# Optimization experiments

Hardware: AMD Instinct MI355X
Metric: run time of the kernel (lower is better)

Reference implementation:

```python
import jax, jax.numpy as jnp
import numpy as np

HEAD_SIZE = 64

def setup_inputs() -> dict:
    key = jax.random.key(0)
    k1, k2, k3, k4 = jax.random.split(key, 4)
    B, T, D = 4, 4096, 768
    x = jax.random.normal(k1, (B, T, D), dtype=jnp.float32)
    Wq = jax.random.normal(k2, (D, HEAD_SIZE), dtype=jnp.float32) * (1.0 / np.sqrt(D))
    Wk = jax.random.normal(k3, (D, HEAD_SIZE), dtype=jnp.float32) * (1.0 / np.sqrt(D))
    Wv = jax.random.normal(k4, (D, HEAD_SIZE), dtype=jnp.float32) * (1.0 / np.sqrt(D))
    return {"x": x, "Wq": Wq, "Wk": Wk, "Wv": Wv}

def reference(x, Wq, Wk, Wv):
    # q,k,v: [B, T, H]
    q = jnp.einsum('btd,dh->bth', x, Wq)
    k = jnp.einsum('btd,dh->bth', x, Wk)
    v = jnp.einsum('btd,dh->bth', x, Wv)
    # scores: [B, T, T]; causal mask via lower-triangular band, -inf elsewhere
    scores = jnp.einsum('bqh,bkh->bqk', q, k)
    T = x.shape[1]
    causal = jnp.tril(jnp.ones((T, T), dtype=bool))  # band_part(ones, -1, 0)
    scores = jnp.where(causal[None, :, :], scores, -jnp.inf)
    attn = jax.nn.softmax(scores / np.sqrt(HEAD_SIZE), axis=-1)
    # dropout is identity in eval mode
    return jnp.einsum('bqk,bkh->bqh', attn, v)
```

## Files before the change

### kernel.cpp

```cpp
#include <hip/hip_runtime.h>
#include <math.h>

typedef __attribute__((ext_vector_type(8))) short short8;
typedef __attribute__((ext_vector_type(4))) float f32x4;
typedef unsigned short ushort_t;

#define TSEQ   4096
#define NBATCH 4
#define DMODEL 768
#define HS     64
#define KSPLIT 8

static __device__ __forceinline__ ushort_t f2bf(float f) {
  union { float f; unsigned u; } v; v.f = f;
  unsigned r = v.u + 0x7fffu + ((v.u >> 16) & 1u);
  return (ushort_t)(r >> 16);
}
static __device__ __forceinline__ float bf2f(ushort_t u) {
  union { unsigned u; float f; } v; v.u = ((unsigned)u) << 16; return v.f;
}

#define MFMA16(a,b,c) __builtin_amdgcn_mfma_f32_16x16x32_bf16((a),(b),(c),0,0,0)

__global__ __launch_bounds__(256) void wprep(
    const float* __restrict__ Wq, const float* __restrict__ Wk,
    const float* __restrict__ Wv, ushort_t* __restrict__ Wt)
{
  __shared__ float lds[64 * 65];
  const int m = blockIdx.x / 12, kc = blockIdx.x % 12, k0 = kc * 64;
  const float* W = (m == 0) ? Wq : (m == 1) ? Wk : Wv;
  const int tid = threadIdx.x;
#pragma unroll
  for (int i = 0; i < 16; i++) {
    const int row = i * 4 + (tid >> 6), col = tid & 63;
    lds[row * 65 + col] = W[(size_t)(k0 + row) * HS + col];
  }
  __syncthreads();
#pragma unroll
  for (int i = 0; i < 16; i++) {
    const int n = i * 4 + (tid >> 6), kk = tid & 63;
    Wt[(size_t)(m * 64 + n) * DMODEL + k0 + kk] = f2bf(lds[kk * 65 + n]);
  }
}

__global__ __launch_bounds__(256, 2) void qkv_mfma(
    const float* __restrict__ x, const ushort_t* __restrict__ Wt,
    ushort_t* __restrict__ q, ushort_t* __restrict__ kO, ushort_t* __restrict__ vT)
{
  __shared__ __align__(16) ushort_t sA[2][32 * 72];
  __shared__ __align__(16) ushort_t sB[2][192 * 64];

  const int tid  = threadIdx.x;
  const int w    = tid >> 6;
  const int lane = tid & 63;
  const int l16  = lane & 15, quad = lane >> 4;
  const int M0   = blockIdx.x * 32;

  const int arow = tid >> 3, acol = (tid & 7) * 8;
  const float* ax = x + (size_t)(M0 + arow) * DMODEL + acol;

  const int bcol_l = lane >> 3;
  const int bkoff  = (((lane & 7) ^ (bcol_l & 7)) << 3);

  f32x4 acc[2][3];
#pragma unroll
  for (int mt = 0; mt < 2; mt++)
#pragma unroll
    for (int nt = 0; nt < 3; nt++) acc[mt][nt] = (f32x4){0.f, 0.f, 0.f, 0.f};

  {
#pragma unroll
    for (int j = 0; j < 6; j++) {
      const int colb = w * 48 + j * 8;
      __builtin_amdgcn_global_load_lds(
          (const __attribute__((address_space(1))) ushort_t*)
              (Wt + (size_t)(colb + bcol_l) * DMODEL + bkoff),
          (__attribute__((address_space(3))) ushort_t*)(&sB[0][colb * 64]),
          16, 0, 0);
    }
    const float4 f0 = *(const float4*)(ax);
    const float4 f1 = *(const float4*)(ax + 4);
    short8 p;
    p[0]=f2bf(f0.x); p[1]=f2bf(f0.y); p[2]=f2bf(f0.z); p[3]=f2bf(f0.w);
    p[4]=f2bf(f1.x); p[5]=f2bf(f1.y); p[6]=f2bf(f1.z); p[7]=f2bf(f1.w);
    *(short8*)(&sA[0][arow * 72 + acol]) = p;
  }

  for (int ks = 0; ks < DMODEL / 64; ks++) {
    const int cur = ks & 1, nxt = cur ^ 1;
    __syncthreads();

    float4 f0n, f1n;
    if (ks < DMODEL / 64 - 1) {
#pragma unroll
      for (int j = 0; j < 6; j++) {
        const int colb = w * 48 + j * 8;
        __builtin_amdgcn_global_load_lds(
            (const __attribute__((address_space(1))) ushort_t*)
                (Wt + (size_t)(colb + bcol_l) * DMODEL + (ks + 1) * 64 + bkoff),
            (__attribute__((address_space(3))) ushort_t*)(&sB[nxt][colb * 64]),
            16, 0, 0);
      }
      f0n = *(const float4*)(ax + (ks + 1) * 64);
      f1n = *(const float4*)(ax + (ks + 1) * 64 + 4);
    }

    const ushort_t* sAc = &sA[cur][0];
    const ushort_t* sBc = &sB[cur][0];
#pragma unroll
    for (int kc = 0; kc < 2; kc++) {
      const short8 a0 = *(const short8*)(sAc + (l16)      * 72 + kc * 32 + quad * 8);
      const short8 a1 = *(const short8*)(sAc + (16 + l16) * 72 + kc * 32 + quad * 8);
      const int kswz = (kc * 32 + quad * 8) ^ ((l16 & 7) << 3);
#pragma unroll
      for (int nt = 0; nt < 3; nt++) {
        const short8 bf =
            *(const short8*)(sBc + (w * 48 + nt * 16 + l16) * 64 + kswz);
        acc[0][nt] = MFMA16(a0, bf, acc[0][nt]);
        acc[1][nt] = MFMA16(a1, bf, acc[1][nt]);
      }
    }

    if (ks < DMODEL / 64 - 1) {
      short8 p;
      p[0]=f2bf(f0n.x); p[1]=f2bf(f0n.y); p[2]=f2bf(f0n.z); p[3]=f2bf(f0n.w);
      p[4]=f2bf(f1n.x); p[5]=f2bf(f1n.y); p[6]=f2bf(f1n.z); p[7]=f2bf(f1n.w);
      *(short8*)(&sA[nxt][arow * 72 + acol]) = p;
    }
  }

#pragma unroll
  for (int mt = 0; mt < 2; mt++)
#pragma unroll
    for (int nt = 0; nt < 3; nt++) {
      const int gnt = w * 3 + nt;
      const int mat = gnt >> 2;
      if (mat == 0) {
        const int col = (gnt & 3) * 16 + l16;
#pragma unroll
        for (int r = 0; r < 4; r++)
          q[(size_t)(M0 + mt * 16 + quad * 4 + r) * HS + col] =
              f2bf(acc[mt][nt][r] * 0.125f);
      } else if (mat == 1) {
        const int cb2 = (gnt & 3) * 2 + (l16 >> 3);
#pragma unroll
        for (int r = 0; r < 4; r++) {
          const int trow  = M0 + mt * 16 + quad * 4 + r;
          const int cphys = ((cb2 ^ (trow & 7)) << 3) | (l16 & 7);
          kO[(size_t)trow * HS + cphys] = f2bf(acc[mt][nt][r]);
        }
      }
    }
  __syncthreads();
  float* vls = (float*)&sA[0][0];
#pragma unroll
  for (int mt = 0; mt < 2; mt++)
#pragma unroll
    for (int nt = 0; nt < 3; nt++) {
      const int gnt = w * 3 + nt;
      if ((gnt >> 2) == 2) {
        const int vcol = (gnt & 3) * 16 + l16;
#pragma unroll
        for (int r = 0; r < 4; r++)
          vls[(mt * 16 + quad * 4 + r) * 65 + vcol] = acc[mt][nt][r];
      }
    }
  __syncthreads();
  const int d = tid >> 2, seg = tid & 3;
  short8 pk;
#pragma unroll
  for (int i = 0; i < 8; i++) pk[i] = (short)f2bf(vls[(seg * 8 + i) * 65 + d]);
  {
    const int t0  = M0 & (TSEQ - 1);
    const int tb  = t0 & ~63;
    const int kb  = ((t0 & 63) >> 3) + seg;
    const int kbp = kb ^ (d & 7);
    *(short8*)(vT + ((size_t)(M0 >> 12) * HS + d) * TSEQ + tb + kbp * 8) = pk;
  }
}

__global__ __launch_bounds__(256, 4) void attn_part(
    const ushort_t* __restrict__ q, const ushort_t* __restrict__ k,
    const ushort_t* __restrict__ vT, float* __restrict__ ML, ushort_t* __restrict__ OP)
{
  __shared__ __align__(16) ushort_t sK[2][64 * 64];
  __shared__ __align__(16) ushort_t sV[2][64 * 64];
  __shared__ __align__(16) ushort_t sP[4][16 * 64];

  const int idx  = blockIdx.x;
  const int s    = idx & 7;
  const int b    = (idx >> 3) & 3;
  const int jp   = idx >> 5;
  const int tid  = threadIdx.x;
  const int w    = tid >> 6;
  const int lane = tid & 63;
  const int l16  = lane & 15, quad = lane >> 4;

  const ushort_t* qg = q  + (size_t)b * TSEQ * HS;
  const ushort_t* kg = k  + (size_t)b * TSEQ * HS;
  const ushort_t* vg = vT + (size_t)b * HS * TSEQ;

  const int srow = lane >> 3;
  const int scol = (lane & 7) * 8;

#pragma unroll
  for (int h = 0; h < 2; h++) {
    const int j  = h ? jp : (63 - jp);
    const int R0 = j * 64 + w * 16;

    const short8 qf0 = *(const short8*)(qg + (size_t)(R0 + l16) * HS +      quad * 8);
    const short8 qf1 = *(const short8*)(qg + (size_t)(R0 + l16) * HS + 32 + quad * 8);

    f32x4 o[4];
#pragma unroll
    for (int dt = 0; dt < 4; dt++) o[dt] = (f32x4){0.f, 0.f, 0.f, 0.f};
    float mrow = -INFINITY, lrow = 0.f;

    const int nkt = j + 1;
    int kt = s, cur = 0;
    if (h) __syncthreads();
    if (kt < nkt) {
      const int k0 = kt * 64;
#pragma unroll
      for (int jj = 0; jj < 2; jj++) {
        const int r0 = w * 16 + jj * 8;
        __builtin_amdgcn_global_load_lds(
            (const __attribute__((address_space(1))) ushort_t*)
                (kg + (size_t)(k0 + r0 + srow) * HS + scol),
            (__attribute__((address_space(3))) ushort_t*)(&sK[0][r0 * 64]),
            16, 0, 0);
        __builtin_amdgcn_global_load_lds(
            (const __attribute__((address_space(1))) ushort_t*)
                (vg + (size_t)(r0 + srow) * TSEQ + k0 + scol),
            (__attribute__((address_space(3))) ushort_t*)(&sV[0][r0 * 64]),
            16, 0, 0);
      }
    }
    for (; kt < nkt; kt += KSPLIT) {
      const int k0 = kt * 64;
      __syncthreads();
      if (kt + KSPLIT < nkt) {
        const int kn = (kt + KSPLIT) * 64;
#pragma unroll
        for (int jj = 0; jj < 2; jj++) {
          const int r0 = w * 16 + jj * 8;
          __builtin_amdgcn_global_load_lds(
              (const __attribute__((address_space(1))) ushort_t*)
                  (kg + (size_t)(kn + r0 + srow) * HS + scol),
              (__attribute__((address_space(3))) ushort_t*)(&sK[cur ^ 1][r0 * 64]),
              16, 0, 0);
          __builtin_amdgcn_global_load_lds(
              (const __attribute__((address_space(1))) ushort_t*)
                  (vg + (size_t)(r0 + srow) * TSEQ + kn + scol),
              (__attribute__((address_space(3))) ushort_t*)(&sV[cur ^ 1][r0 * 64]),
              16, 0, 0);
        }
      }
      const ushort_t* sKc = &sK[cur][0];
      const ushort_t* sVc = &sV[cur][0];
      const int sw = (l16 & 7) << 3;

      f32x4 sT[4];
      __builtin_amdgcn_s_setprio(1);
#pragma unroll
      for (int ct = 0; ct < 4; ct++) {
        sT[ct] = (f32x4){0.f, 0.f, 0.f, 0.f};
        const short8 kfa = *(const short8*)(sKc + (ct * 16 + l16) * 64 + ((quad * 8)      ^ sw));
        const short8 kfb = *(const short8*)(sKc + (ct * 16 + l16) * 64 + ((32 + quad * 8) ^ sw));
        sT[ct] = MFMA16(kfa, qf0, sT[ct]);
        sT[ct] = MFMA16(kfb, qf1, sT[ct]);
      }
      __builtin_amdgcn_s_setprio(0);
      if (k0 + 63 > R0) {
        const int qrow = R0 + l16;
#pragma unroll
        for (int ct = 0; ct < 4; ct++)
#pragma unroll
          for (int r = 0; r < 4; r++)
            sT[ct][r] = (k0 + ct * 16 + quad * 4 + r <= qrow) ? sT[ct][r] : -INFINITY;
      }
      float tm = -INFINITY;
#pragma unroll
      for (int ct = 0; ct < 4; ct++)
#pragma unroll
        for (int r = 0; r < 4; r++) tm = fmaxf(tm, sT[ct][r]);
      tm = fmaxf(tm, __shfl_xor(tm, 16));
      tm = fmaxf(tm, __shfl_xor(tm, 32));
      const float mn = fmaxf(mrow, tm);
      const float al = __expf(mrow - mn);
      mrow = mn;
      float ps = 0.f;
#pragma unroll
      for (int ct = 0; ct < 4; ct++)
#pragma unroll
        for (int r = 0; r < 4; r++) { sT[ct][r] = __expf(sT[ct][r] - mn); ps += sT[ct][r]; }
      ps += __shfl_xor(ps, 16);
      ps += __shfl_xor(ps, 32);
      lrow = lrow * al + ps;
      ushort_t* Pw = &sP[w][0];
#pragma unroll
      for (int ct = 0; ct < 4; ct++) {
        ushort4 pk;
        pk.x = f2bf(sT[ct][0]); pk.y = f2bf(sT[ct][1]);
        pk.z = f2bf(sT[ct][2]); pk.w = f2bf(sT[ct][3]);
        const int pb = (ct * 2 + (quad >> 1)) ^ (l16 & 7);
        *(ushort4*)(Pw + l16 * 64 + pb * 8 + (quad & 1) * 4) = pk;
      }
      float alo[4];
#pragma unroll
      for (int r = 0; r < 4; r++) alo[r] = __shfl(al, quad * 4 + r);
#pragma unroll
      for (int dt = 0; dt < 4; dt++)
#pragma unroll
        for (int r = 0; r < 4; r++) o[dt][r] *= alo[r];
      const short8 pf0 = *(const short8*)(Pw + l16 * 64 + (((quad)     ^ (l16 & 7)) << 3));
      const short8 pf1 = *(const short8*)(Pw + l16 * 64 + (((4 + quad) ^ (l16 & 7)) << 3));
      __builtin_amdgcn_s_setprio(1);
#pragma unroll
      for (int dt = 0; dt < 4; dt++) {
        const short8 vfa = *(const short8*)(sVc + (dt * 16 + l16) * 64 + ((quad * 8)      ^ sw));
        const short8 vfb = *(const short8*)(sVc + (dt * 16 + l16) * 64 + ((32 + quad * 8) ^ sw));
        o[dt] = MFMA16(pf0, vfa, o[dt]);
        o[dt] = MFMA16(pf1, vfb, o[dt]);
      }
      __builtin_amdgcn_s_setprio(0);
      cur ^= 1;
    }

    const size_t base = ((size_t)(b * KSPLIT + s) * TSEQ);
    if (quad == 0) {
      ML[(base + R0 + l16) * 2 + 0] = mrow;
      ML[(base + R0 + l16) * 2 + 1] = lrow;
    }
#pragma unroll
    for (int dt = 0; dt < 4; dt++)
#pragma unroll
      for (int r = 0; r < 4; r++)
        OP[(base + R0 + quad * 4 + r) * HS + dt * 16 + l16] = f2bf(o[dt][r]);
  }
}

__global__ __launch_bounds__(256) void attn_merge(
    const float* __restrict__ ML, const ushort_t* __restrict__ OP,
    float* __restrict__ out)
{
  const int row = blockIdx.x * 16 + (threadIdx.x >> 4);
  const int b   = row >> 12, t = row & (TSEQ - 1);
  const int d0  = (threadIdx.x & 15) * 4;
  float m[KSPLIT], l[KSPLIT];
  float M = -INFINITY;
#pragma unroll
  for (int ss = 0; ss < KSPLIT; ss++) {
    const size_t i = ((size_t)(b * KSPLIT + ss) * TSEQ + t);
    m[ss] = ML[i * 2]; l[ss] = ML[i * 2 + 1];
    M = fmaxf(M, m[ss]);
  }
  float den = 0.f;
  float4 num = make_float4(0.f, 0.f, 0.f, 0.f);
#pragma unroll
  for (int ss = 0; ss < KSPLIT; ss++) {
    const float a = __expf(m[ss] - M);
    den += l[ss] * a;
    const size_t i = ((size_t)(b * KSPLIT + ss) * TSEQ + t);
    const ushort4 u = *(const ushort4*)(OP + i * HS + d0);
    num.x += a * bf2f(u.x); num.y += a * bf2f(u.y);
    num.z += a * bf2f(u.z); num.w += a * bf2f(u.w);
  }
  const float inv = 1.f / den;
  *(float4*)(out + (size_t)row * HS + d0) =
      make_float4(num.x * inv, num.y * inv, num.z * inv, num.w * inv);
}

extern "C" void kernel_launch(void* const* d_in, const int* in_sizes, int n_in,
                              void* d_out, int out_size, void* d_ws, size_t ws_size,
                              hipStream_t stream) {
  const float* x  = (const float*)d_in[0];
  const float* Wq = (const float*)d_in[1];
  const float* Wk = (const float*)d_in[2];
  const float* Wv = (const float*)d_in[3];
  float* out = (float*)d_out;

  char* ws = (char*)d_ws;
  ushort_t* Wt = (ushort_t*)ws;
  ushort_t* qb = (ushort_t*)(ws + 294912);
  ushort_t* kb = (ushort_t*)(ws + 294912 + 2097152);
  ushort_t* vb = (ushort_t*)(ws + 294912 + 2 * 2097152);
  float*    ml = (float*)   (ws + 294912 + 3 * 2097152);
  ushort_t* op = (ushort_t*)(ws + 294912 + 3 * 2097152 + 1048576);

  wprep<<<36, 256, 0, stream>>>(Wq, Wk, Wv, Wt);
  qkv_mfma<<<(NBATCH * TSEQ) / 32, 256, 0, stream>>>(x, Wt, qb, kb, vb);
  attn_part<<<32 * NBATCH * KSPLIT, 256, 0, stream>>>(qb, kb, vb, ml, op);
  attn_merge<<<1024, 256, 0, stream>>>(ml, op, out);
}
```

Baseline: 131.3 us.

## Fuse all four kernels into one cooperative kernel with grid syncs

```diff
diff --git a/kernel.cpp b/kernel.cpp
--- a/kernel.cpp
+++ b/kernel.cpp
@@ -1,5 +1,8 @@
 #include <hip/hip_runtime.h>
+#include <hip/hip_cooperative_groups.h>
 #include <math.h>
+
+namespace cg = cooperative_groups;
 
 typedef __attribute__((ext_vector_type(8))) short short8;
 typedef __attribute__((ext_vector_type(4))) float f32x4;
@@ -9,7 +12,7 @@
 #define NBATCH 4
 #define DMODEL 768
 #define HS     64
-#define KSPLIT 8
+#define KS     4
 
 static __device__ __forceinline__ ushort_t f2bf(float f) {
   union { float f; unsigned u; } v; v.f = f;
@@ -22,353 +25,360 @@
 
 #define MFMA16(a,b,c) __builtin_amdgcn_mfma_f32_16x16x32_bf16((a),(b),(c),0,0,0)
 
-__global__ __launch_bounds__(256) void wprep(
-    const float* __restrict__ Wq, const float* __restrict__ Wk,
-    const float* __restrict__ Wv, ushort_t* __restrict__ Wt)
+__global__ __launch_bounds__(256, 2) void fused_all(
+    const float* __restrict__ x,  const float* __restrict__ Wq,
+    const float* __restrict__ Wk, const float* __restrict__ Wv,
+    ushort_t* __restrict__ Wt, ushort_t* __restrict__ q,
+    ushort_t* __restrict__ kO, ushort_t* __restrict__ vT,
+    float* __restrict__ ML, ushort_t* __restrict__ OP,
+    float* __restrict__ out)
 {
-  __shared__ float lds[64 * 65];
-  const int m = blockIdx.x / 12, kc = blockIdx.x % 12, k0 = kc * 64;
-  const float* W = (m == 0) ? Wq : (m == 1) ? Wk : Wv;
-  const int tid = threadIdx.x;
-#pragma unroll
-  for (int i = 0; i < 16; i++) {
-    const int row = i * 4 + (tid >> 6), col = tid & 63;
-    lds[row * 65 + col] = W[(size_t)(k0 + row) * HS + col];
-  }
-  __syncthreads();
-#pragma unroll
-  for (int i = 0; i < 16; i++) {
-    const int n = i * 4 + (tid >> 6), kk = tid & 63;
-    Wt[(size_t)(m * 64 + n) * DMODEL + k0 + kk] = f2bf(lds[kk * 65 + n]);
-  }
-}
-
-__global__ __launch_bounds__(256, 2) void qkv_mfma(
-    const float* __restrict__ x, const ushort_t* __restrict__ Wt,
-    ushort_t* __restrict__ q, ushort_t* __restrict__ kO, ushort_t* __restrict__ vT)
-{
-  __shared__ __align__(16) ushort_t sA[2][32 * 72];
-  __shared__ __align__(16) ushort_t sB[2][192 * 64];
+  __shared__ __align__(16) ushort_t smem[29184];
+
+  cg::grid_group grid = cg::this_grid();
 
   const int tid  = threadIdx.x;
+  const int bid  = blockIdx.x;
   const int w    = tid >> 6;
   const int lane = tid & 63;
   const int l16  = lane & 15, quad = lane >> 4;
-  const int M0   = blockIdx.x * 32;
-
-  const int arow = tid >> 3, acol = (tid & 7) * 8;
-  const float* ax = x + (size_t)(M0 + arow) * DMODEL + acol;
-
-  const int bcol_l = lane >> 3;
-  const int bkoff  = (((lane & 7) ^ (bcol_l & 7)) << 3);
-
-  f32x4 acc[2][3];
-#pragma unroll
-  for (int mt = 0; mt < 2; mt++)
-#pragma unroll
-    for (int nt = 0; nt < 3; nt++) acc[mt][nt] = (f32x4){0.f, 0.f, 0.f, 0.f};
+
+  if (bid < 36) {
+    float* lds = (float*)smem;
+    const int m = bid / 12, kc = bid % 12, k0 = kc * 64;
+    const float* W = (m == 0) ? Wq : (m == 1) ? Wk : Wv;
+#pragma unroll
+    for (int i = 0; i < 16; i++) {
+      const int row = i * 4 + (tid >> 6), col = tid & 63;
+      lds[row * 65 + col] = W[(size_t)(k0 + row) * HS + col];
+    }
+    __syncthreads();
+#pragma unroll
+    for (int i = 0; i < 16; i++) {
+      const int n = i * 4 + (tid >> 6), kk = tid & 63;
+      Wt[(size_t)(m * 64 + n) * DMODEL + k0 + kk] = f2bf(lds[kk * 65 + n]);
+    }
+  }
+  grid.sync();
 
   {
-#pragma unroll
-    for (int j = 0; j < 6; j++) {
-      const int colb = w * 48 + j * 8;
-      __builtin_amdgcn_global_load_lds(
-          (const __attribute__((address_space(1))) ushort_t*)
-              (Wt + (size_t)(colb + bcol_l) * DMODEL + bkoff),
-          (__attribute__((address_space(3))) ushort_t*)(&sB[0][colb * 64]),
-          16, 0, 0);
-    }
-    const float4 f0 = *(const float4*)(ax);
-    const float4 f1 = *(const float4*)(ax + 4);
-    short8 p;
-    p[0]=f2bf(f0.x); p[1]=f2bf(f0.y); p[2]=f2bf(f0.z); p[3]=f2bf(f0.w);
-    p[4]=f2bf(f1.x); p[5]=f2bf(f1.y); p[6]=f2bf(f1.z); p[7]=f2bf(f1.w);
-    *(short8*)(&sA[0][arow * 72 + acol]) = p;
-  }
-
-  for (int ks = 0; ks < DMODEL / 64; ks++) {
-    const int cur = ks & 1, nxt = cur ^ 1;
-    __syncthreads();
-
-    float4 f0n, f1n;
-    if (ks < DMODEL / 64 - 1) {
+    ushort_t* sA = smem;
+    ushort_t* sB = smem + 2 * 32 * 72;
+    const int M0 = bid * 32;
+
+    const int arow = tid >> 3, acol = (tid & 7) * 8;
+    const float* ax = x + (size_t)(M0 + arow) * DMODEL + acol;
+
+    const int bcol_l = lane >> 3;
+    const int bkoff  = (((lane & 7) ^ (bcol_l & 7)) << 3);
+
+    f32x4 acc[2][3];
+#pragma unroll
+    for (int mt = 0; mt < 2; mt++)
+#pragma unroll
+      for (int nt = 0; nt < 3; nt++) acc[mt][nt] = (f32x4){0.f, 0.f, 0.f, 0.f};
+
+    {
 #pragma unroll
       for (int j = 0; j < 6; j++) {
         const int colb = w * 48 + j * 8;
         __builtin_amdgcn_global_load_lds(
             (const __attribute__((address_space(1))) ushort_t*)
-                (Wt + (size_t)(colb + bcol_l) * DMODEL + (ks + 1) * 64 + bkoff),
-            (__attribute__((address_space(3))) ushort_t*)(&sB[nxt][colb * 64]),
+                (Wt + (size_t)(colb + bcol_l) * DMODEL + bkoff),
+            (__attribute__((address_space(3))) ushort_t*)(&sB[colb * 64]),
             16, 0, 0);
       }
-      f0n = *(const float4*)(ax + (ks + 1) * 64);
-      f1n = *(const float4*)(ax + (ks + 1) * 64 + 4);
-    }
-
-    const ushort_t* sAc = &sA[cur][0];
-    const ushort_t* sBc = &sB[cur][0];
-#pragma unroll
-    for (int kc = 0; kc < 2; kc++) {
-      const short8 a0 = *(const short8*)(sAc + (l16)      * 72 + kc * 32 + quad * 8);
-      const short8 a1 = *(const short8*)(sAc + (16 + l16) * 72 + kc * 32 + quad * 8);
-      const int kswz = (kc * 32 + quad * 8) ^ ((l16 & 7) << 3);
+      const float4 f0 = *(const float4*)(ax);
+      const float4 f1 = *(const float4*)(ax + 4);
+      short8 p;
+      p[0]=f2bf(f0.x); p[1]=f2bf(f0.y); p[2]=f2bf(f0.z); p[3]=f2bf(f0.w);
+      p[4]=f2bf(f1.x); p[5]=f2bf(f1.y); p[6]=f2bf(f1.z); p[7]=f2bf(f1.w);
+      *(short8*)(&sA[arow * 72 + acol]) = p;
+    }
+
+    for (int ks = 0; ks < DMODEL / 64; ks++) {
+      const int cur = ks & 1, nxt = cur ^ 1;
+      __syncthreads();
+
+      float4 f0n, f1n;
+      if (ks < DMODEL / 64 - 1) {
+#pragma unroll
+        for (int j = 0; j < 6; j++) {
+          const int colb = w * 48 + j * 8;
+          __builtin_amdgcn_global_load_lds(
+              (const __attribute__((address_space(1))) ushort_t*)
+                  (Wt + (size_t)(colb + bcol_l) * DMODEL + (ks + 1) * 64 + bkoff),
+              (__attribute__((address_space(3))) ushort_t*)
+                  (&sB[nxt * 192 * 64 + colb * 64]),
+              16, 0, 0);
+        }
+        f0n = *(const float4*)(ax + (ks + 1) * 64);
+        f1n = *(const float4*)(ax + (ks + 1) * 64 + 4);
+      }
+
+      const ushort_t* sAc = &sA[cur * 32 * 72];
+      const ushort_t* sBc = &sB[cur * 192 * 64];
+#pragma unroll
+      for (int kc = 0; kc < 2; kc++) {
+        const short8 a0 = *(const short8*)(sAc + (l16)      * 72 + kc * 32 + quad * 8);
+        const short8 a1 = *(const short8*)(sAc + (16 + l16) * 72 + kc * 32 + quad * 8);
+        const int kswz = (kc * 32 + quad * 8) ^ ((l16 & 7) << 3);
+#pragma unroll
+        for (int nt = 0; nt < 3; nt++) {
+          const short8 bf =
+              *(const short8*)(sBc + (w * 48 + nt * 16 + l16) * 64 + kswz);
+          acc[0][nt] = MFMA16(a0, bf, acc[0][nt]);
+          acc[1][nt] = MFMA16(a1, bf, acc[1][nt]);
+        }
+      }
+
+      if (ks < DMODEL / 64 - 1) {
+        short8 p;
+        p[0]=f2bf(f0n.x); p[1]=f2bf(f0n.y); p[2]=f2bf(f0n.z); p[3]=f2bf(f0n.w);
+        p[4]=f2bf(f1n.x); p[5]=f2bf(f1n.y); p[6]=f2bf(f1n.z); p[7]=f2bf(f1n.w);
+        *(short8*)(&sA[nxt * 32 * 72 + arow * 72 + acol]) = p;
+      }
+    }
+
+#pragma unroll
+    for (int mt = 0; mt < 2; mt++)
 #pragma unroll
       for (int nt = 0; nt < 3; nt++) {
-        const short8 bf =
-            *(const short8*)(sBc + (w * 48 + nt * 16 + l16) * 64 + kswz);
-        acc[0][nt] = MFMA16(a0, bf, acc[0][nt]);
-        acc[1][nt] = MFMA16(a1, bf, acc[1][nt]);
-      }
-    }
-
-    if (ks < DMODEL / 64 - 1) {
-      short8 p;
-      p[0]=f2bf(f0n.x); p[1]=f2bf(f0n.y); p[2]=f2bf(f0n.z); p[3]=f2bf(f0n.w);
-      p[4]=f2bf(f1n.x); p[5]=f2bf(f1n.y); p[6]=f2bf(f1n.z); p[7]=f2bf(f1n.w);
-      *(short8*)(&sA[nxt][arow * 72 + acol]) = p;
+        const int gnt = w * 3 + nt;
+        const int mat = gnt >> 2;
+        if (mat == 0) {
+          const int col = (gnt & 3) * 16 + l16;
+#pragma unroll
+          for (int r = 0; r < 4; r++)
+            q[(size_t)(M0 + mt * 16 + quad * 4 + r) * HS + col] =
+                f2bf(acc[mt][nt][r] * 0.125f);
+        } else if (mat == 1) {
+          const int cb2 = (gnt & 3) * 2 + (l16 >> 3);
+#pragma unroll
+          for (int r = 0; r < 4; r++) {
+            const int trow  = M0 + mt * 16 + quad * 4 + r;
+            const int cphys = ((cb2 ^ (trow & 7)) << 3) | (l16 & 7);
+            kO[(size_t)trow * HS + cphys] = f2bf(acc[mt][nt][r]);
+          }
+        }
+      }
+    __syncthreads();
+    float* vls = (float*)smem;
+#pragma unroll
+    for (int mt = 0; mt < 2; mt++)
+#pragma unroll
+      for (int nt = 0; nt < 3; nt++) {
+        const int gnt = w * 3 + nt;
+        if ((gnt >> 2) == 2) {
+          const int vcol = (gnt & 3) * 16 + l16;
+#pragma unroll
+          for (int r = 0; r < 4; r++)
+            vls[(mt * 16 + quad * 4 + r) * 65 + vcol] = acc[mt][nt][r];
+        }
+      }
+    __syncthreads();
+    const int d = tid >> 2, seg = tid & 3;
+    short8 pk;
+#pragma unroll
+    for (int i = 0; i < 8; i++) pk[i] = (short)f2bf(vls[(seg * 8 + i) * 65 + d]);
+    {
+      const int t0  = M0 & (TSEQ - 1);
+      const int tb  = t0 & ~63;
+      const int kb  = ((t0 & 63) >> 3) + seg;
+      const int kbp = kb ^ (d & 7);
+      *(short8*)(vT + ((size_t)(M0 >> 12) * HS + d) * TSEQ + tb + kbp * 8) = pk;
     }
   }
-
-#pragma unroll
-  for (int mt = 0; mt < 2; mt++)
-#pragma unroll
-    for (int nt = 0; nt < 3; nt++) {
-      const int gnt = w * 3 + nt;
-      const int mat = gnt >> 2;
-      if (mat == 0) {
-        const int col = (gnt & 3) * 16 + l16;
-#pragma unroll
-        for (int r = 0; r < 4; r++)
-          q[(size_t)(M0 + mt * 16 + quad * 4 + r) * HS + col] =
-              f2bf(acc[mt][nt][r] * 0.125f);
-      } else if (mat == 1) {
-        const int cb2 = (gnt & 3) * 2 + (l16 >> 3);
-#pragma unroll
-        for (int r = 0; r < 4; r++) {
-          const int trow  = M0 + mt * 16 + quad * 4 + r;
-          const int cphys = ((cb2 ^ (trow & 7)) << 3) | (l16 & 7);
-          kO[(size_t)trow * HS + cphys] = f2bf(acc[mt][nt][r]);
-        }
-      }
-    }
-  __syncthreads();
-  float* vls = (float*)&sA[0][0];
-#pragma unroll
-  for (int mt = 0; mt < 2; mt++)
-#pragma unroll
-    for (int nt = 0; nt < 3; nt++) {
-      const int gnt = w * 3 + nt;
-      if ((gnt >> 2) == 2) {
-        const int vcol = (gnt & 3) * 16 + l16;
-#pragma unroll
-        for (int r = 0; r < 4; r++)
-          vls[(mt * 16 + quad * 4 + r) * 65 + vcol] = acc[mt][nt][r];
-      }
-    }
-  __syncthreads();
-  const int d = tid >> 2, seg = tid & 3;
-  short8 pk;
-#pragma unroll
-  for (int i = 0; i < 8; i++) pk[i] = (short)f2bf(vls[(seg * 8 + i) * 65 + d]);
+  grid.sync();
+
   {
-    const int t0  = M0 & (TSEQ - 1);
-    const int tb  = t0 & ~63;
-    const int kb  = ((t0 & 63) >> 3) + seg;
-    const int kbp = kb ^ (d & 7);
-    *(short8*)(vT + ((size_t)(M0 >> 12) * HS + d) * TSEQ + tb + kbp * 8) = pk;
-  }
-}
-
-__global__ __launch_bounds__(256, 4) void attn_part(
-    const ushort_t* __restrict__ q, const ushort_t* __restrict__ k,
-    const ushort_t* __restrict__ vT, float* __restrict__ ML, ushort_t* __restrict__ OP)
-{
-  __shared__ __align__(16) ushort_t sK[2][64 * 64];
-  __shared__ __align__(16) ushort_t sV[2][64 * 64];
-  __shared__ __align__(16) ushort_t sP[4][16 * 64];
-
-  const int idx  = blockIdx.x;
-  const int s    = idx & 7;
-  const int b    = (idx >> 3) & 3;
-  const int jp   = idx >> 5;
-  const int tid  = threadIdx.x;
-  const int w    = tid >> 6;
-  const int lane = tid & 63;
-  const int l16  = lane & 15, quad = lane >> 4;
-
-  const ushort_t* qg = q  + (size_t)b * TSEQ * HS;
-  const ushort_t* kg = k  + (size_t)b * TSEQ * HS;
-  const ushort_t* vg = vT + (size_t)b * HS * TSEQ;
-
-  const int srow = lane >> 3;
-  const int scol = (lane & 7) * 8;
-
-#pragma unroll
-  for (int h = 0; h < 2; h++) {
-    const int j  = h ? jp : (63 - jp);
-    const int R0 = j * 64 + w * 16;
-
-    const short8 qf0 = *(const short8*)(qg + (size_t)(R0 + l16) * HS +      quad * 8);
-    const short8 qf1 = *(const short8*)(qg + (size_t)(R0 + l16) * HS + 32 + quad * 8);
-
-    f32x4 o[4];
-#pragma unroll
-    for (int dt = 0; dt < 4; dt++) o[dt] = (f32x4){0.f, 0.f, 0.f, 0.f};
-    float mrow = -INFINITY, lrow = 0.f;
-
-    const int nkt = j + 1;
-    int kt = s, cur = 0;
-    if (h) __syncthreads();
-    if (kt < nkt) {
-      const int k0 = kt * 64;
-#pragma unroll
-      for (int jj = 0; jj < 2; jj++) {
-        const int r0 = w * 16 + jj * 8;
-        __builtin_amdgcn_global_load_lds(
-            (const __attribute__((address_space(1))) ushort_t*)
-                (kg + (size_t)(k0 + r0 + srow) * HS + scol),
-            (__attribute__((address_space(3))) ushort_t*)(&sK[0][r0 * 64]),
-            16, 0, 0);
-        __builtin_amdgcn_global_load_lds(
-            (const __attribute__((address_space(1))) ushort_t*)
-                (vg + (size_t)(r0 + srow) * TSEQ + k0 + scol),
-            (__attribute__((address_space(3))) ushort_t*)(&sV[0][r0 * 64]),
-            16, 0, 0);
-      }
-    }
-    for (; kt < nkt; kt += KSPLIT) {
-      const int k0 = kt * 64;
-      __syncthreads();
-      if (kt + KSPLIT < nkt) {
-        const int kn = (kt + KSPLIT) * 64;
+    ushort_t* sK = smem;
+    ushort_t* sV = smem + 2 * 64 * 64;
+    ushort_t* sP = smem + 4 * 64 * 64;
+
+    const int s  = bid & 3;
+    const int b  = (bid >> 2) & 3;
+    const int jp = bid >> 4;
+
+    const ushort_t* qg = q  + (size_t)b * TSEQ * HS;
+    const ushort_t* kg = kO + (size_t)b * TSEQ * HS;
+    const ushort_t* vg = vT + (size_t)b * HS * TSEQ;
+
+    const int srow = lane >> 3;
+    const int scol = (lane & 7) * 8;
+
+#pragma unroll
+    for (int h = 0; h < 2; h++) {
+      const int j  = h ? jp : (63 - jp);
+      const int R0 = j * 64 + w * 16;
+
+      const short8 qf0 = *(const short8*)(qg + (size_t)(R0 + l16) * HS +      quad * 8);
+      const short8 qf1 = *(const short8*)(qg + (size_t)(R0 + l16) * HS + 32 + quad * 8);
+
+      f32x4 o[4];
+#pragma unroll
+      for (int dt = 0; dt < 4; dt++) o[dt] = (f32x4){0.f, 0.f, 0.f, 0.f};
+      float mrow = -INFINITY, lrow = 0.f;
+
+      const int nkt = j + 1;
+      int kt = s, cur = 0;
+      if (h) __syncthreads();
+      if (kt < nkt) {
+        const int k0 = kt * 64;
 #pragma unroll
         for (int jj = 0; jj < 2; jj++) {
           const int r0 = w * 16 + jj * 8;
           __builtin_amdgcn_global_load_lds(
               (const __attribute__((address_space(1))) ushort_t*)
-                  (kg + (size_t)(kn + r0 + srow) * HS + scol),
-              (__attribute__((address_space(3))) ushort_t*)(&sK[cur ^ 1][r0 * 64]),
+                  (kg + (size_t)(k0 + r0 + srow) * HS + scol),
+              (__attribute__((address_space(3))) ushort_t*)(&sK[r0 * 64]),
               16, 0, 0);
           __builtin_amdgcn_global_load_lds(
               (const __attribute__((address_space(1))) ushort_t*)
-                  (vg + (size_t)(r0 + srow) * TSEQ + kn + scol),
-              (__attribute__((address_space(3))) ushort_t*)(&sV[cur ^ 1][r0 * 64]),
+                  (vg + (size_t)(r0 + srow) * TSEQ + k0 + scol),
+              (__attribute__((address_space(3))) ushort_t*)(&sV[r0 * 64]),
               16, 0, 0);
         }
       }
-      const ushort_t* sKc = &sK[cur][0];
-      const ushort_t* sVc = &sV[cur][0];
-      const int sw = (l16 & 7) << 3;
-
-      f32x4 sT[4];
-      __builtin_amdgcn_s_setprio(1);
-#pragma unroll
-      for (int ct = 0; ct < 4; ct++) {
-        sT[ct] = (f32x4){0.f, 0.f, 0.f, 0.f};
-        const short8 kfa = *(const short8*)(sKc + (ct * 16 + l16) * 64 + ((quad * 8)      ^ sw));
-        const short8 kfb = *(const short8*)(sKc + (ct * 16 + l16) * 64 + ((32 + quad * 8) ^ sw));
-        sT[ct] = MFMA16(kfa, qf0, sT[ct]);
-        sT[ct] = MFMA16(kfb, qf1, sT[ct]);
-      }
-      __builtin_amdgcn_s_setprio(0);
-      if (k0 + 63 > R0) {
-        const int qrow = R0 + l16;
+      for (; kt < nkt; kt += KS) {
+        const int k0 = kt * 64;
+        __syncthreads();
+        if (kt + KS < nkt) {
+          const int kn = (kt + KS) * 64;
+#pragma unroll
+          for (int jj = 0; jj < 2; jj++) {
+            const int r0 = w * 16 + jj * 8;
+            __builtin_amdgcn_global_load_lds(
+                (const __attribute__((address_space(1))) ushort_t*)
+                    (kg + (size_t)(kn + r0 + srow) * HS + scol),
+                (__attribute__((address_space(3))) ushort_t*)
+                    (&sK[(cur ^ 1) * 64 * 64 + r0 * 64]),
+                16, 0, 0);
+            __builtin_amdgcn_global_load_lds(
+                (const __attribute__((address_space(1))) ushort_t*)
+                    (vg + (size_t)(r0 + srow) * TSEQ + kn + scol),
+                (__attribute__((address_space(3))) ushort_t*)
+                    (&sV[(cur ^ 1) * 64 * 64 + r0 * 64]),
+                16, 0, 0);
+          }
+        }
+        const ushort_t* sKc = &sK[cur * 64 * 64];
+        const ushort_t* sVc = &sV[cur * 64 * 64];
+        const int sw = (l16 & 7) << 3;
+
+        f32x4 sT[4];
+        __builtin_amdgcn_s_setprio(1);
+#pragma unroll
+        for (int ct = 0; ct < 4; ct++) {
+          sT[ct] = (f32x4){0.f, 0.f, 0.f, 0.f};
+          const short8 kfa = *(const short8*)(sKc + (ct * 16 + l16) * 64 + ((quad * 8)      ^ sw));
+          const short8 kfb = *(const short8*)(sKc + (ct * 16 + l16) * 64 + ((32 + quad * 8) ^ sw));
+          sT[ct] = MFMA16(kfa, qf0, sT[ct]);
+          sT[ct] = MFMA16(kfb, qf1, sT[ct]);
+        }
+        __builtin_amdgcn_s_setprio(0);
+        if (k0 + 63 > R0) {
+          const int qrow = R0 + l16;
+#pragma unroll
+          for (int ct = 0; ct < 4; ct++)
+#pragma unroll
+            for (int r = 0; r < 4; r++)
+              sT[ct][r] = (k0 + ct * 16 + quad * 4 + r <= qrow) ? sT[ct][r] : -INFINITY;
+        }
+        float tm = -INFINITY;
 #pragma unroll
         for (int ct = 0; ct < 4; ct++)
 #pragma unroll
-          for (int r = 0; r < 4; r++)
-            sT[ct][r] = (k0 + ct * 16 + quad * 4 + r <= qrow) ? sT[ct][r] : -INFINITY;
-      }
-      float tm = -INFINITY;
-#pragma unroll
-      for (int ct = 0; ct < 4; ct++)
-#pragma unroll
-        for (int r = 0; r < 4; r++) tm = fmaxf(tm, sT[ct][r]);
-      tm = fmaxf(tm, __shfl_xor(tm, 16));
-      tm = fmaxf(tm, __shfl_xor(tm, 32));
-      const float mn = fmaxf(mrow, tm);
-      const float al = __expf(mrow - mn);
-      mrow = mn;
-      float ps = 0.f;
-#pragma unroll
-      for (int ct = 0; ct < 4; ct++)
-#pragma unroll
-        for (int r = 0; r < 4; r++) { sT[ct][r] = __expf(sT[ct][r] - mn); ps += sT[ct][r]; }
-      ps += __shfl_xor(ps, 16);
-      ps += __shfl_xor(ps, 32);
-      lrow = lrow * al + ps;
-      ushort_t* Pw = &sP[w][0];
-#pragma unroll
-      for (int ct = 0; ct < 4; ct++) {
-        ushort4 pk;
-        pk.x = f2bf(sT[ct][0]); pk.y = f2bf(sT[ct][1]);
-        pk.z = f2bf(sT[ct][2]); pk.w = f2bf(sT[ct][3]);
-        const int pb = (ct * 2 + (quad >> 1)) ^ (l16 & 7);
-        *(ushort4*)(Pw + l16 * 64 + pb * 8 + (quad & 1) * 4) = pk;
-      }
-      float alo[4];
-#pragma unroll
-      for (int r = 0; r < 4; r++) alo[r] = __shfl(al, quad * 4 + r);
+          for (int r = 0; r < 4; r++) tm = fmaxf(tm, sT[ct][r]);
+        tm = fmaxf(tm, __shfl_xor(tm, 16));
+        tm = fmaxf(tm, __shfl_xor(tm, 32));
+        const float mn = fmaxf(mrow, tm);
+        const float al = __expf(mrow - mn);
+        mrow = mn;
+        float ps = 0.f;
+#pragma unroll
+        for (int ct = 0; ct < 4; ct++)
+#pragma unroll
+          for (int r = 0; r < 4; r++) { sT[ct][r] = __expf(sT[ct][r] - mn); ps += sT[ct][r]; }
+        ps += __shfl_xor(ps, 16);
+        ps += __shfl_xor(ps, 32);
+        lrow = lrow * al + ps;
+
+        ushort_t* Pw = &sP[w * 16 * 64];
+#pragma unroll
+        for (int ct = 0; ct < 4; ct++) {
+          ushort4 pk;
+          pk.x = f2bf(sT[ct][0]); pk.y = f2bf(sT[ct][1]);
+          pk.z = f2bf(sT[ct][2]); pk.w = f2bf(sT[ct][3]);
+          const int pb = (ct * 2 + (quad >> 1)) ^ (l16 & 7);
+          *(ushort4*)(Pw + l16 * 64 + pb * 8 + (quad & 1) * 4) = pk;
+        }
+        float alo[4];
+#pragma unroll
+        for (int r = 0; r < 4; r++) alo[r] = __shfl(al, quad * 4 + r);
+#pragma unroll
+        for (int dt = 0; dt < 4; dt++)
+#pragma unroll
+          for (int r = 0; r < 4; r++) o[dt][r] *= alo[r];
+        const short8 pf0 = *(const short8*)(Pw + l16 * 64 + (((quad)     ^ (l16 & 7)) << 3));
+        const short8 pf1 = *(const short8*)(Pw + l16 * 64 + (((4 + quad) ^ (l16 & 7)) << 3));
+        __builtin_amdgcn_s_setprio(1);
+#pragma unroll
+        for (int dt = 0; dt < 4; dt++) {
+          const short8 vfa = *(const short8*)(sVc + (dt * 16 + l16) * 64 + ((quad * 8)      ^ sw));
+          const short8 vfb = *(const short8*)(sVc + (dt * 16 + l16) * 64 + ((32 + quad * 8) ^ sw));
+          o[dt] = MFMA16(pf0, vfa, o[dt]);
+          o[dt] = MFMA16(pf1, vfb, o[dt]);
+        }
+        __builtin_amdgcn_s_setprio(0);
+        cur ^= 1;
+      }
+
+      const size_t base = ((size_t)(b * KS + s) * TSEQ);
+      if (quad == 0) {
+        ML[(base + R0 + l16) * 2 + 0] = mrow;
+        ML[(base + R0 + l16) * 2 + 1] = lrow;
+      }
 #pragma unroll
       for (int dt = 0; dt < 4; dt++)
 #pragma unroll
-        for (int r = 0; r < 4; r++) o[dt][r] *= alo[r];
-      const short8 pf0 = *(const short8*)(Pw + l16 * 64 + (((quad)     ^ (l16 & 7)) << 3));
-      const short8 pf1 = *(const short8*)(Pw + l16 * 64 + (((4 + quad) ^ (l16 & 7)) << 3));
-      __builtin_amdgcn_s_setprio(1);
-#pragma unroll
-      for (int dt = 0; dt < 4; dt++) {
-        const short8 vfa = *(const short8*)(sVc + (dt * 16 + l16) * 64 + ((quad * 8)      ^ sw));
-        const short8 vfb = *(const short8*)(sVc + (dt * 16 + l16) * 64 + ((32 + quad * 8) ^ sw));
-        o[dt] = MFMA16(pf0, vfa, o[dt]);
-        o[dt] = MFMA16(pf1, vfb, o[dt]);
-      }
-      __builtin_amdgcn_s_setprio(0);
-      cur ^= 1;
-    }
-
-    const size_t base = ((size_t)(b * KSPLIT + s) * TSEQ);
-    if (quad == 0) {
-      ML[(base + R0 + l16) * 2 + 0] = mrow;
-      ML[(base + R0 + l16) * 2 + 1] = lrow;
-    }
-#pragma unroll
-    for (int dt = 0; dt < 4; dt++)
-#pragma unroll
-      for (int r = 0; r < 4; r++)
-        OP[(base + R0 + quad * 4 + r) * HS + dt * 16 + l16] = f2bf(o[dt][r]);
+        for (int r = 0; r < 4; r++)
+          OP[(base + R0 + quad * 4 + r) * HS + dt * 16 + l16] = f2bf(o[dt][r]);
+    }
   }
-}
-
-__global__ __launch_bounds__(256) void attn_merge(
-    const float* __restrict__ ML, const ushort_t* __restrict__ OP,
-    float* __restrict__ out)
-{
-  const int row = blockIdx.x * 16 + (threadIdx.x >> 4);
-  const int b   = row >> 12, t = row & (TSEQ - 1);
-  const int d0  = (threadIdx.x & 15) * 4;
-  float m[KSPLIT], l[KSPLIT];
-  float M = -INFINITY;
-#pragma unroll
-  for (int ss = 0; ss < KSPLIT; ss++) {
-    const size_t i = ((size_t)(b * KSPLIT + ss) * TSEQ + t);
-    m[ss] = ML[i * 2]; l[ss] = ML[i * 2 + 1];
-    M = fmaxf(M, m[ss]);
+  grid.sync();
+
+  {
+    const int row = bid * 32 + (tid >> 3);
+    const int b   = row >> 12, t = row & (TSEQ - 1);
+    const int d0  = (tid & 7) * 8;
+    float m4[KS], l4[KS];
+    float M = -INFINITY;
+#pragma unroll
+    for (int ss = 0; ss < KS; ss++) {
+      const size_t i = ((size_t)(b * KS + ss) * TSEQ + t);
+      m4[ss] = ML[i * 2]; l4[ss] = ML[i * 2 + 1];
+      M = fmaxf(M, m4[ss]);
+    }
+    float den = 0.f;
+    float n0=0.f,n1=0.f,n2=0.f,n3=0.f,n4=0.f,n5=0.f,n6=0.f,n7=0.f;
+#pragma unroll
+    for (int ss = 0; ss < KS; ss++) {
+      const float a = __expf(m4[ss] - M);
+      den += l4[ss] * a;
+      const size_t i = ((size_t)(b * KS + ss) * TSEQ + t);
+      const ushort4 u0 = *(const ushort4*)(OP + i * HS + d0);
+      const ushort4 u1 = *(const ushort4*)(OP + i * HS + d0 + 4);
+      n0 += a * bf2f(u0.x); n1 += a * bf2f(u0.y);
+      n2 += a * bf2f(u0.z); n3 += a * bf2f(u0.w);
+      n4 += a * bf2f(u1.x); n5 += a * bf2f(u1.y);
+      n6 += a * bf2f(u1.z); n7 += a * bf2f(u1.w);
+    }
+    const float inv = 1.f / den;
+    float* op = out + (size_t)row * HS + d0;
+    *(float4*)(op)     = make_float4(n0 * inv, n1 * inv, n2 * inv, n3 * inv);
+    *(float4*)(op + 4) = make_float4(n4 * inv, n5 * inv, n6 * inv, n7 * inv);
   }
-  float den = 0.f;
-  float4 num = make_float4(0.f, 0.f, 0.f, 0.f);
-#pragma unroll
-  for (int ss = 0; ss < KSPLIT; ss++) {
-    const float a = __expf(m[ss] - M);
-    den += l[ss] * a;
-    const size_t i = ((size_t)(b * KSPLIT + ss) * TSEQ + t);
-    const ushort4 u = *(const ushort4*)(OP + i * HS + d0);
-    num.x += a * bf2f(u.x); num.y += a * bf2f(u.y);
-    num.z += a * bf2f(u.z); num.w += a * bf2f(u.w);
-  }
-  const float inv = 1.f / den;
-  *(float4*)(out + (size_t)row * HS + d0) =
-      make_float4(num.x * inv, num.y * inv, num.z * inv, num.w * inv);
 }
 
 extern "C" void kernel_launch(void* const* d_in, const int* in_sizes, int n_in,
@@ -386,10 +396,11 @@
   ushort_t* kb = (ushort_t*)(ws + 294912 + 2097152);
   ushort_t* vb = (ushort_t*)(ws + 294912 + 2 * 2097152);
   float*    ml = (float*)   (ws + 294912 + 3 * 2097152);
-  ushort_t* op = (ushort_t*)(ws + 294912 + 3 * 2097152 + 1048576);
-
-  wprep<<<36, 256, 0, stream>>>(Wq, Wk, Wv, Wt);
-  qkv_mfma<<<(NBATCH * TSEQ) / 32, 256, 0, stream>>>(x, Wt, qb, kb, vb);
-  attn_part<<<32 * NBATCH * KSPLIT, 256, 0, stream>>>(qb, kb, vb, ml, op);
-  attn_merge<<<1024, 256, 0, stream>>>(ml, op, out);
+  ushort_t* op = (ushort_t*)(ws + 294912 + 3 * 2097152 + 524288);
+
+  void* args[] = {(void*)&x,  (void*)&Wq, (void*)&Wk, (void*)&Wv,
+                  (void*)&Wt, (void*)&qb, (void*)&kb, (void*)&vb,
+                  (void*)&ml, (void*)&op, (void*)&out};
+  hipLaunchCooperativeKernel((const void*)fused_all, dim3(512), dim3(256),
+                             args, 0, stream);
 }
```

Measured after the change: 310.8 us. +136.7%, slower.

## Double QKV projection M-tile to 64 rows with 512 threads; widen merge loads

Applied to the files above, without the earlier changes.

```diff
diff --git a/kernel.cpp b/kernel.cpp
--- a/kernel.cpp
+++ b/kernel.cpp
@@ -43,18 +43,19 @@
   }
 }
 
-__global__ __launch_bounds__(256, 2) void qkv_mfma(
+__global__ __launch_bounds__(512, 1) void qkv_mfma(
     const float* __restrict__ x, const ushort_t* __restrict__ Wt,
     ushort_t* __restrict__ q, ushort_t* __restrict__ kO, ushort_t* __restrict__ vT)
 {
-  __shared__ __align__(16) ushort_t sA[2][32 * 72];
+  __shared__ __align__(16) ushort_t sA[2][64 * 72];
   __shared__ __align__(16) ushort_t sB[2][192 * 64];
 
   const int tid  = threadIdx.x;
   const int w    = tid >> 6;
+  const int wm   = w >> 2, wn = w & 3;
   const int lane = tid & 63;
   const int l16  = lane & 15, quad = lane >> 4;
-  const int M0   = blockIdx.x * 32;
+  const int M0   = blockIdx.x * 64;
 
   const int arow = tid >> 3, acol = (tid & 7) * 8;
   const float* ax = x + (size_t)(M0 + arow) * DMODEL + acol;
@@ -70,8 +71,8 @@
 
   {
 #pragma unroll
-    for (int j = 0; j < 6; j++) {
-      const int colb = w * 48 + j * 8;
+    for (int j = 0; j < 3; j++) {
+      const int colb = w * 24 + j * 8;
       __builtin_amdgcn_global_load_lds(
           (const __attribute__((address_space(1))) ushort_t*)
               (Wt + (size_t)(colb + bcol_l) * DMODEL + bkoff),
@@ -93,8 +94,8 @@
     float4 f0n, f1n;
     if (ks < DMODEL / 64 - 1) {
 #pragma unroll
-      for (int j = 0; j < 6; j++) {
-        const int colb = w * 48 + j * 8;
+      for (int j = 0; j < 3; j++) {
+        const int colb = w * 24 + j * 8;
         __builtin_amdgcn_global_load_lds(
             (const __attribute__((address_space(1))) ushort_t*)
                 (Wt + (size_t)(colb + bcol_l) * DMODEL + (ks + 1) * 64 + bkoff),
@@ -109,13 +110,13 @@
     const ushort_t* sBc = &sB[cur][0];
 #pragma unroll
     for (int kc = 0; kc < 2; kc++) {
-      const short8 a0 = *(const short8*)(sAc + (l16)      * 72 + kc * 32 + quad * 8);
-      const short8 a1 = *(const short8*)(sAc + (16 + l16) * 72 + kc * 32 + quad * 8);
+      const short8 a0 = *(const short8*)(sAc + (wm * 32 + l16)      * 72 + kc * 32 + quad * 8);
+      const short8 a1 = *(const short8*)(sAc + (wm * 32 + 16 + l16) * 72 + kc * 32 + quad * 8);
       const int kswz = (kc * 32 + quad * 8) ^ ((l16 & 7) << 3);
 #pragma unroll
       for (int nt = 0; nt < 3; nt++) {
         const short8 bf =
-            *(const short8*)(sBc + (w * 48 + nt * 16 + l16) * 64 + kswz);
+            *(const short8*)(sBc + (wn * 48 + nt * 16 + l16) * 64 + kswz);
         acc[0][nt] = MFMA16(a0, bf, acc[0][nt]);
         acc[1][nt] = MFMA16(a1, bf, acc[1][nt]);
       }
@@ -133,19 +134,19 @@
   for (int mt = 0; mt < 2; mt++)
 #pragma unroll
     for (int nt = 0; nt < 3; nt++) {
-      const int gnt = w * 3 + nt;
+      const int gnt = wn * 3 + nt;
       const int mat = gnt >> 2;
       if (mat == 0) {
         const int col = (gnt & 3) * 16 + l16;
 #pragma unroll
         for (int r = 0; r < 4; r++)
-          q[(size_t)(M0 + mt * 16 + quad * 4 + r) * HS + col] =
+          q[(size_t)(M0 + wm * 32 + mt * 16 + quad * 4 + r) * HS + col] =
               f2bf(acc[mt][nt][r] * 0.125f);
       } else if (mat == 1) {
         const int cb2 = (gnt & 3) * 2 + (l16 >> 3);
 #pragma unroll
         for (int r = 0; r < 4; r++) {
-          const int trow  = M0 + mt * 16 + quad * 4 + r;
+          const int trow  = M0 + wm * 32 + mt * 16 + quad * 4 + r;
           const int cphys = ((cb2 ^ (trow & 7)) << 3) | (l16 & 7);
           kO[(size_t)trow * HS + cphys] = f2bf(acc[mt][nt][r]);
         }
@@ -157,24 +158,22 @@
   for (int mt = 0; mt < 2; mt++)
 #pragma unroll
     for (int nt = 0; nt < 3; nt++) {
-      const int gnt = w * 3 + nt;
+      const int gnt = wn * 3 + nt;
       if ((gnt >> 2) == 2) {
         const int vcol = (gnt & 3) * 16 + l16;
 #pragma unroll
         for (int r = 0; r < 4; r++)
-          vls[(mt * 16 + quad * 4 + r) * 65 + vcol] = acc[mt][nt][r];
+          vls[(wm * 32 + mt * 16 + quad * 4 + r) * 65 + vcol] = acc[mt][nt][r];
       }
     }
   __syncthreads();
-  const int d = tid >> 2, seg = tid & 3;
+  const int d = tid >> 3, seg = tid & 7;
   short8 pk;
 #pragma unroll
   for (int i = 0; i < 8; i++) pk[i] = (short)f2bf(vls[(seg * 8 + i) * 65 + d]);
   {
-    const int t0  = M0 & (TSEQ - 1);
-    const int tb  = t0 & ~63;
-    const int kb  = ((t0 & 63) >> 3) + seg;
-    const int kbp = kb ^ (d & 7);
+    const int tb  = M0 & (TSEQ - 1);
+    const int kbp = seg ^ (d & 7);
     *(short8*)(vT + ((size_t)(M0 >> 12) * HS + d) * TSEQ + tb + kbp * 8) = pk;
   }
 }
@@ -344,9 +343,9 @@
     const float* __restrict__ ML, const ushort_t* __restrict__ OP,
     float* __restrict__ out)
 {
-  const int row = blockIdx.x * 16 + (threadIdx.x >> 4);
+  const int row = blockIdx.x * 32 + (threadIdx.x >> 3);
   const int b   = row >> 12, t = row & (TSEQ - 1);
-  const int d0  = (threadIdx.x & 15) * 4;
+  const int d0  = (threadIdx.x & 7) * 8;
   float m[KSPLIT], l[KSPLIT];
   float M = -INFINITY;
 #pragma unroll
@@ -356,19 +355,22 @@
     M = fmaxf(M, m[ss]);
   }
   float den = 0.f;
-  float4 num = make_float4(0.f, 0.f, 0.f, 0.f);
+  float n0=0.f,n1=0.f,n2=0.f,n3=0.f,n4=0.f,n5=0.f,n6=0.f,n7=0.f;
 #pragma unroll
   for (int ss = 0; ss < KSPLIT; ss++) {
     const float a = __expf(m[ss] - M);
     den += l[ss] * a;
     const size_t i = ((size_t)(b * KSPLIT + ss) * TSEQ + t);
-    const ushort4 u = *(const ushort4*)(OP + i * HS + d0);
-    num.x += a * bf2f(u.x); num.y += a * bf2f(u.y);
-    num.z += a * bf2f(u.z); num.w += a * bf2f(u.w);
+    const short8 u = *(const short8*)(OP + i * HS + d0);
+    n0 += a * bf2f((ushort_t)u[0]); n1 += a * bf2f((ushort_t)u[1]);
+    n2 += a * bf2f((ushort_t)u[2]); n3 += a * bf2f((ushort_t)u[3]);
+    n4 += a * bf2f((ushort_t)u[4]); n5 += a * bf2f((ushort_t)u[5]);
+    n6 += a * bf2f((ushort_t)u[6]); n7 += a * bf2f((ushort_t)u[7]);
   }
   const float inv = 1.f / den;
-  *(float4*)(out + (size_t)row * HS + d0) =
-      make_float4(num.x * inv, num.y * inv, num.z * inv, num.w * inv);
+  float* op = out + (size_t)row * HS + d0;
+  *(float4*)(op)     = make_float4(n0 * inv, n1 * inv, n2 * inv, n3 * inv);
+  *(float4*)(op + 4) = make_float4(n4 * inv, n5 * inv, n6 * inv, n7 * inv);
 }
 
 extern "C" void kernel_launch(void* const* d_in, const int* in_sizes, int n_in,
@@ -389,7 +391,7 @@
   ushort_t* op = (ushort_t*)(ws + 294912 + 3 * 2097152 + 1048576);
 
   wprep<<<36, 256, 0, stream>>>(Wq, Wk, Wv, Wt);
-  qkv_mfma<<<(NBATCH * TSEQ) / 32, 256, 0, stream>>>(x, Wt, qb, kb, vb);
+  qkv_mfma<<<(NBATCH * TSEQ) / 64, 512, 0, stream>>>(x, Wt, qb, kb, vb);
   attn_part<<<32 * NBATCH * KSPLIT, 256, 0, stream>>>(qb, kb, vb, ml, op);
-  attn_merge<<<1024, 256, 0, stream>>>(ml, op, out);
-}
+  attn_merge<<<512, 256, 0, stream>>>(ml, op, out);
+}
```

Result: faster. 128.5 us (-2.1%).
